# Kernel optimization log

Measured on AMD Instinct MI355X. Metric: run time of the kernel, lower is better.

Reference implementation:

```python
import jax, jax.numpy as jnp
import numpy as np

N, E, H, PIN, PEIN, POUT, L = 50000, 800000, 128, 16, 8, 8, 4
EPS = 1e-7


def setup_inputs() -> dict:
    key = jax.random.key(0)
    ks = jax.random.split(key, 24)
    f = jax.random.normal
    inp = {
        'x': f(ks[0], (N, PIN), jnp.float32),
        'edge_attr': f(ks[1], (E, PEIN), jnp.float32),
        'edge_index': jax.random.randint(ks[2], (2, E), 0, N, jnp.int32),
        # encoders
        'node_W': f(ks[3], (PIN, H)) * (1.0 / np.sqrt(PIN)),
        'node_b': jnp.zeros((H,)),
        'edge_W': f(ks[4], (PEIN, H)) * (1.0 / np.sqrt(PEIN)),
        'edge_b': jnp.zeros((H,)),
        # GENConv params per layer (stacked over L): MLP Linear(H,2H)->LN->ReLU->Linear(2H,H), temp t
        'W1': f(ks[5], (L, H, 2 * H)) * (1.0 / np.sqrt(H)),
        'b1': jnp.zeros((L, 2 * H)),
        'g1': jnp.ones((L, 2 * H)),
        'be1': jnp.zeros((L, 2 * H)),
        'W2': f(ks[6], (L, 2 * H, H)) * (1.0 / np.sqrt(2 * H)),
        'b2': jnp.zeros((L, H)),
        't': jnp.ones((L,)),
        # DeepGCNLayer LayerNorms
        'ng': jnp.ones((L, H)),
        'nb': jnp.zeros((L, H)),
        # output head
        'out_W': f(ks[7], (H, POUT)) * (1.0 / np.sqrt(H)),
        'out_b': jnp.zeros((POUT,)),
    }
    return inp


def _layernorm(x, g, b):
    mu = jnp.mean(x, -1, keepdims=True)
    v = jnp.mean(jnp.square(x - mu), -1, keepdims=True)
    return (x - mu) * jax.lax.rsqrt(v + 1e-5) * g + b


def reference(x, edge_attr, edge_index, node_W, node_b, edge_W, edge_b,
              W1, b1, g1, be1, W2, b2, t, ng, nb, out_W, out_b):
    src, dst = edge_index[0], edge_index[1]

    def genconv(h, e, i):
        # message: relu(x_j + edge_attr) + eps   [E, H]
        msg = jax.nn.relu(h[src] + e) + EPS
        # softmax aggregation over edges per destination node, temperature t[i]
        s = msg * t[i]
        m = jax.ops.segment_max(s, dst, num_segments=N)  # [N, H]
        w = jnp.exp(s - m[dst])
        denom = jax.ops.segment_sum(w, dst, num_segments=N)
        agg = jax.ops.segment_sum(msg * w, dst, num_segments=N)
        agg = jnp.where(denom > 0, agg / jnp.maximum(denom, EPS), 0.0)
        # root add, then 2-layer MLP (Linear -> LN -> ReLU -> Linear)
        z = agg + h
        z = jax.nn.relu(_layernorm(z @ W1[i] + b1[i], g1[i], be1[i]))
        return z @ W2[i] + b2[i]

    h = x @ node_W + node_b                      # node encoder
    e = jax.nn.sigmoid(edge_attr @ edge_W + edge_b)  # edge encoder
    h = genconv(h, e, 0)                         # layers[0].conv only
    for i in range(1, L):                        # res+ blocks
        z = jax.nn.relu(_layernorm(h, ng[i], nb[i]))
        h = h + genconv(z, e, i)
    h = jax.nn.relu(_layernorm(h, ng[0], nb[0]))  # layers[0] norm+act; dropout=eval identity
    return h @ out_W + out_b
```

## Files before the change

kernel.cpp:

```cpp
#include <hip/hip_runtime.h>
#include <hip/hip_bf16.h>

#define NN 50000
#define NE 800000
#define HH 128
#define PIN_ 16
#define PEIN_ 8
#define POUT_ 8
#define LAYERS_ 4
#define EPSM 1e-7f

typedef __bf16 bf16x8 __attribute__((ext_vector_type(8)));
typedef float f32x4 __attribute__((ext_vector_type(4)));

__device__ inline unsigned short f2bf(float f) {
  unsigned int u = __float_as_uint(f);
  u += 0x7FFFu + ((u >> 16) & 1u);
  return (unsigned short)(u >> 16);
}
__device__ inline unsigned int packbf(float lo, float hi) {
  return (unsigned int)f2bf(lo) | ((unsigned int)f2bf(hi) << 16);
}
__device__ inline float bflo(unsigned int p) { return __uint_as_float(p << 16); }
__device__ inline float bfhi(unsigned int p) { return __uint_as_float(p & 0xFFFF0000u); }


__global__ void count_deg_kernel(const int* __restrict__ dst, int* __restrict__ deg) {
  int i = blockIdx.x * blockDim.x + threadIdx.x;
  if (i < NE) atomicAdd(&deg[dst[i]], 1);
}

__global__ __launch_bounds__(1024) void scan_kernel(const int* __restrict__ deg,
                                                    int* __restrict__ row_ptr,
                                                    int* __restrict__ cursor, int n) {
  __shared__ int wsum[16];
  __shared__ int carry_s;
  int t = threadIdx.x;
  int lane = t & 63, wv = t >> 6;
  if (t == 0) carry_s = 0;
  __syncthreads();
  for (int base = 0; base < n; base += 1024) {
    int i = base + t;
    int v = (i < n) ? deg[i] : 0;
    int x = v;
#pragma unroll
    for (int off = 1; off < 64; off <<= 1) {
      int y = __shfl_up(x, off, 64);
      if (lane >= off) x += y;
    }
    if (lane == 63) wsum[wv] = x;
    __syncthreads();
    if (wv == 0 && lane < 16) {
      int s = wsum[lane];
#pragma unroll
      for (int off = 1; off < 16; off <<= 1) {
        int y = __shfl_up(s, off, 16);
        if (lane >= off) s += y;
      }
      wsum[lane] = s;
    }
    __syncthreads();
    int waveExcl = (wv > 0) ? wsum[wv - 1] : 0;
    int carry = carry_s;
    int excl = carry + waveExcl + x - v;
    if (i < n) { row_ptr[i] = excl; cursor[i] = excl; }
    __syncthreads();
    if (t == 1023) carry_s = carry + wsum[15];
    __syncthreads();
  }
  if (t == 0) row_ptr[n] = carry_s;
}

__global__ void scatter_kernel(const int* __restrict__ src, const int* __restrict__ dst,
                               int* __restrict__ cursor, int2* __restrict__ csr) {
  int i = blockIdx.x * blockDim.x + threadIdx.x;
  if (i < NE) {
    int d = dst[i];
    int pos = atomicAdd(&cursor[d], 1);
    csr[pos] = make_int2(src[i], i);
  }
}


__global__ __launch_bounds__(256) void prep_weights_kernel(
    const float* __restrict__ W1, const float* __restrict__ W2,
    unsigned short* __restrict__ W1Tp, unsigned short* __restrict__ W2T) {
  int idx = blockIdx.x * 256 + threadIdx.x;
  if (idx >= LAYERS_ * 256 * 128) return;
  int l = idx >> 15, r = idx & 32767;
  int n = r >> 7, p = r & 127;
  int k = (p >> 1) + ((p & 1) << 6);
  W1Tp[idx] = f2bf(W1[(l << 15) + k * 256 + n]);
  int c = r >> 8, kk = r & 255;
  W2T[idx] = f2bf(W2[(l << 15) + kk * 128 + c]);
}


__global__ __launch_bounds__(64) void node_enc_kernel(const float* __restrict__ x,
                                                      const float* __restrict__ W,
                                                      const float* __restrict__ b,
                                                      float* __restrict__ h,
                                                      unsigned int* __restrict__ hbp) {
  __shared__ float xs[8 * PIN_];
  int f = threadIdx.x;
  float w0[PIN_], w1[PIN_];
#pragma unroll
  for (int k = 0; k < PIN_; ++k) {
    w0[k] = W[k * HH + f];
    w1[k] = W[k * HH + f + 64];
  }
  float b0 = b[f], b1c = b[f + 64];
  int base = blockIdx.x * 8;
  xs[f] = x[(size_t)base * PIN_ + f];
  xs[f + 64] = x[(size_t)base * PIN_ + f + 64];
  __syncthreads();
#pragma unroll
  for (int r = 0; r < 8; ++r) {
    float a0 = b0, a1 = b1c;
#pragma unroll
    for (int k = 0; k < PIN_; ++k) {
      a0 = fmaf(xs[r * PIN_ + k], w0[k], a0);
      a1 = fmaf(xs[r * PIN_ + k], w1[k], a1);
    }
    h[(size_t)(base + r) * HH + f] = a0;
    h[(size_t)(base + r) * HH + f + 64] = a1;
    hbp[(size_t)(base + r) * 64 + f] = packbf(a0, a1);
  }
}


struct AggState { float d0, d1, a0, a1; };

__device__ __forceinline__ void edge_step(float4 A, float4 B, unsigned int zp,
                                          const float* ew0, const float* ew1,
                                          float eb0, float eb1, float t,
                                          AggState& st) {
  float acc0 = eb0, acc1 = eb1;
  acc0 = fmaf(A.x, ew0[0], acc0); acc0 = fmaf(A.y, ew0[1], acc0);
  acc0 = fmaf(A.z, ew0[2], acc0); acc0 = fmaf(A.w, ew0[3], acc0);
  acc0 = fmaf(B.x, ew0[4], acc0); acc0 = fmaf(B.y, ew0[5], acc0);
  acc0 = fmaf(B.z, ew0[6], acc0); acc0 = fmaf(B.w, ew0[7], acc0);
  acc1 = fmaf(A.x, ew1[0], acc1); acc1 = fmaf(A.y, ew1[1], acc1);
  acc1 = fmaf(A.z, ew1[2], acc1); acc1 = fmaf(A.w, ew1[3], acc1);
  acc1 = fmaf(B.x, ew1[4], acc1); acc1 = fmaf(B.y, ew1[5], acc1);
  acc1 = fmaf(B.z, ew1[6], acc1); acc1 = fmaf(B.w, ew1[7], acc1);
  float e0 = __builtin_amdgcn_rcpf(1.f + __expf(-acc0));
  float e1 = __builtin_amdgcn_rcpf(1.f + __expf(-acc1));
  float msg0 = fmaxf(bflo(zp) + e0, 0.f) + EPSM;
  float msg1 = fmaxf(bfhi(zp) + e1, 0.f) + EPSM;
  float w0 = __expf(msg0 * t), w1 = __expf(msg1 * t);
  st.d0 += w0; st.d1 += w1;
  st.a0 = fmaf(msg0, w0, st.a0);
  st.a1 = fmaf(msg1, w1, st.a1);
}

__global__ __launch_bounds__(256) void aggregate_kernel(
    const int* __restrict__ row_ptr, const int2* __restrict__ csr,
    const float* __restrict__ edge_attr, const float* __restrict__ edge_W,
    const float* __restrict__ edge_b, const unsigned int* __restrict__ zpk,
    const float* __restrict__ t_all, int layer, unsigned int* __restrict__ upk) {
  int wv = threadIdx.x >> 6, lane = threadIdx.x & 63;
  int n = blockIdx.x * 4 + wv;
  if (n >= NN) return;
  float ew0[PEIN_], ew1[PEIN_];
#pragma unroll
  for (int k = 0; k < PEIN_; ++k) {
    ew0[k] = edge_W[k * HH + lane];
    ew1[k] = edge_W[k * HH + lane + 64];
  }
  float eb0 = edge_b[lane], eb1 = edge_b[lane + 64];
  float t = t_all[layer];
  int beg = row_ptr[n], end = row_ptr[n + 1];
  unsigned int zs = zpk[(size_t)n * 64 + lane];
  AggState st = {0.f, 0.f, 0.f, 0.f};

  int p = beg;
  for (; p + 4 <= end; p += 4) {
    int2 se0 = csr[p + 0];
    int2 se1 = csr[p + 1];
    int2 se2 = csr[p + 2];
    int2 se3 = csr[p + 3];
    const float4* e0p = (const float4*)(edge_attr + (size_t)se0.y * PEIN_);
    const float4* e1p = (const float4*)(edge_attr + (size_t)se1.y * PEIN_);
    const float4* e2p = (const float4*)(edge_attr + (size_t)se2.y * PEIN_);
    const float4* e3p = (const float4*)(edge_attr + (size_t)se3.y * PEIN_);
    float4 A0 = e0p[0], B0 = e0p[1];
    float4 A1 = e1p[0], B1 = e1p[1];
    float4 A2 = e2p[0], B2 = e2p[1];
    float4 A3 = e3p[0], B3 = e3p[1];
    unsigned int z0 = zpk[(size_t)se0.x * 64 + lane];
    unsigned int z1 = zpk[(size_t)se1.x * 64 + lane];
    unsigned int z2 = zpk[(size_t)se2.x * 64 + lane];
    unsigned int z3 = zpk[(size_t)se3.x * 64 + lane];
    edge_step(A0, B0, z0, ew0, ew1, eb0, eb1, t, st);
    edge_step(A1, B1, z1, ew0, ew1, eb0, eb1, t, st);
    edge_step(A2, B2, z2, ew0, ew1, eb0, eb1, t, st);
    edge_step(A3, B3, z3, ew0, ew1, eb0, eb1, t, st);
  }
  for (; p < end; ++p) {
    int2 se = csr[p];
    const float4* ep = (const float4*)(edge_attr + (size_t)se.y * PEIN_);
    float4 A = ep[0], B = ep[1];
    unsigned int zp = zpk[(size_t)se.x * 64 + lane];
    edge_step(A, B, zp, ew0, ew1, eb0, eb1, t, st);
  }

  float agg0 = (st.d0 > 0.f) ? st.a0 / fmaxf(st.d0, EPSM) : 0.f;
  float agg1 = (st.d1 > 0.f) ? st.a1 / fmaxf(st.d1, EPSM) : 0.f;
  float u0 = agg0 + bflo(zs);
  float u1 = agg1 + bfhi(zs);
  upk[(size_t)n * 64 + lane] = packbf(u0, u1);
}


__global__ __launch_bounds__(256) void mlp_fused_kernel(
    const unsigned int* __restrict__ upk,
    const unsigned short* __restrict__ W1Tp,
    const float* __restrict__ b1v, const float* __restrict__ g1v,
    const float* __restrict__ be1v,
    const unsigned short* __restrict__ W2T,
    const float* __restrict__ b2v,
    const float* __restrict__ res,
    const float* __restrict__ ngv, const float* __restrict__ nbv,
    float* __restrict__ hout, float* __restrict__ zoutf,
    unsigned int* __restrict__ zbp) {
  __shared__ __align__(16) unsigned short Tlds[4 * 4096];
  int wv = threadIdx.x >> 6, lane = threadIdx.x & 63;
  int gw = blockIdx.x * 4 + wv;
  if (gw >= NN / 16) return;
  int row0 = gw * 16;
  int l15 = lane & 15, qg = lane >> 4;
  int co = 4 * qg;
  int sx = (l15 & 7) << 3;
  unsigned short* tl = Tlds + wv * 4096;

  const unsigned short* ub =
      (const unsigned short*)upk + (size_t)(row0 + l15) * HH + qg * 8;
  bf16x8 ufr[4];
#pragma unroll
  for (int kb = 0; kb < 4; ++kb) ufr[kb] = *(const bf16x8*)(ub + kb * 32);
  f32x4 acc1[16];
#pragma unroll
  for (int nb = 0; nb < 16; ++nb) acc1[nb] = (f32x4){0.f, 0.f, 0.f, 0.f};
#pragma unroll
  for (int nb = 0; nb < 16; ++nb) {
#pragma unroll
    for (int kb = 0; kb < 4; ++kb) {
      bf16x8 wf = *(const bf16x8*)(W1Tp + (size_t)(nb * 16 + l15) * HH + kb * 32 + qg * 8);
      acc1[nb] = __builtin_amdgcn_mfma_f32_16x16x32_bf16(wf, ufr[kb], acc1[nb], 0, 0, 0);
    }
  }

  float sum1 = 0.f;
#pragma unroll
  for (int nb = 0; nb < 16; ++nb) {
    float4 bq = *(const float4*)(b1v + nb * 16 + co);
    acc1[nb][0] += bq.x; acc1[nb][1] += bq.y;
    acc1[nb][2] += bq.z; acc1[nb][3] += bq.w;
    sum1 += acc1[nb][0] + acc1[nb][1] + acc1[nb][2] + acc1[nb][3];
  }
  sum1 += __shfl_xor(sum1, 16, 64);
  sum1 += __shfl_xor(sum1, 32, 64);
  float mu1 = sum1 * (1.f / 256.f);
  float sq1 = 0.f;
#pragma unroll
  for (int nb = 0; nb < 16; ++nb)
#pragma unroll
    for (int i = 0; i < 4; ++i) {
      float d = acc1[nb][i] - mu1;
      sq1 = fmaf(d, d, sq1);
    }
  sq1 += __shfl_xor(sq1, 16, 64);
  sq1 += __shfl_xor(sq1, 32, 64);
  float rstd1 = rsqrtf(sq1 * (1.f / 256.f) + 1e-5f);
#pragma unroll
  for (int nb = 0; nb < 16; ++nb) {
    float4 gq = *(const float4*)(g1v + nb * 16 + co);
    float4 eq = *(const float4*)(be1v + nb * 16 + co);
    float t0 = fmaxf(fmaf((acc1[nb][0] - mu1) * rstd1, gq.x, eq.x), 0.f);
    float t1 = fmaxf(fmaf((acc1[nb][1] - mu1) * rstd1, gq.y, eq.y), 0.f);
    float t2 = fmaxf(fmaf((acc1[nb][2] - mu1) * rstd1, gq.z, eq.z), 0.f);
    float t3 = fmaxf(fmaf((acc1[nb][3] - mu1) * rstd1, gq.w, eq.w), 0.f);
    int ad = l15 * 256 + ((nb * 16 + co) ^ sx);
    *(uint2*)(tl + ad) = make_uint2(packbf(t0, t1), packbf(t2, t3));
  }

  f32x4 acc2[8];
#pragma unroll
  for (int nc = 0; nc < 8; ++nc) acc2[nc] = (f32x4){0.f, 0.f, 0.f, 0.f};
#pragma unroll
  for (int kb = 0; kb < 8; ++kb) {
    bf16x8 tf = *(const bf16x8*)(tl + l15 * 256 + ((kb * 32 + qg * 8) ^ sx));
#pragma unroll
    for (int nc = 0; nc < 8; ++nc) {
      bf16x8 wf = *(const bf16x8*)(W2T + (size_t)(nc * 16 + l15) * 256 + kb * 32 + qg * 8);
      acc2[nc] = __builtin_amdgcn_mfma_f32_16x16x32_bf16(wf, tf, acc2[nc], 0, 0, 0);
    }
  }

  size_t rb = (size_t)(row0 + l15) * HH;
  float sum2 = 0.f;
#pragma unroll
  for (int nc = 0; nc < 8; ++nc) {
    float4 bq = *(const float4*)(b2v + nc * 16 + co);
    acc2[nc][0] += bq.x; acc2[nc][1] += bq.y;
    acc2[nc][2] += bq.z; acc2[nc][3] += bq.w;
    if (res) {
      float4 rq = *(const float4*)(res + rb + nc * 16 + co);
      acc2[nc][0] += rq.x; acc2[nc][1] += rq.y;
      acc2[nc][2] += rq.z; acc2[nc][3] += rq.w;
    }
    *(float4*)(hout + rb + nc * 16 + co) =
        make_float4(acc2[nc][0], acc2[nc][1], acc2[nc][2], acc2[nc][3]);
    sum2 += acc2[nc][0] + acc2[nc][1] + acc2[nc][2] + acc2[nc][3];
  }
  sum2 += __shfl_xor(sum2, 16, 64);
  sum2 += __shfl_xor(sum2, 32, 64);
  float mu2 = sum2 * (1.f / 128.f);
  float sq2 = 0.f;
#pragma unroll
  for (int nc = 0; nc < 8; ++nc)
#pragma unroll
    for (int i = 0; i < 4; ++i) {
      float d = acc2[nc][i] - mu2;
      sq2 = fmaf(d, d, sq2);
    }
  sq2 += __shfl_xor(sq2, 16, 64);
  sq2 += __shfl_xor(sq2, 32, 64);
  float rstd2 = rsqrtf(sq2 * (1.f / 128.f) + 1e-5f);
#pragma unroll
  for (int nc = 0; nc < 8; ++nc) {
    float4 gq = *(const float4*)(ngv + nc * 16 + co);
    float4 eq = *(const float4*)(nbv + nc * 16 + co);
    acc2[nc][0] = fmaxf(fmaf((acc2[nc][0] - mu2) * rstd2, gq.x, eq.x), 0.f);
    acc2[nc][1] = fmaxf(fmaf((acc2[nc][1] - mu2) * rstd2, gq.y, eq.y), 0.f);
    acc2[nc][2] = fmaxf(fmaf((acc2[nc][2] - mu2) * rstd2, gq.z, eq.z), 0.f);
    acc2[nc][3] = fmaxf(fmaf((acc2[nc][3] - mu2) * rstd2, gq.w, eq.w), 0.f);
  }
  if (zoutf) {
#pragma unroll
    for (int nc = 0; nc < 8; ++nc)
      *(float4*)(zoutf + rb + nc * 16 + co) =
          make_float4(acc2[nc][0], acc2[nc][1], acc2[nc][2], acc2[nc][3]);
  }
#pragma unroll
  for (int nc = 0; nc < 4; ++nc) {
    *(uint4*)(zbp + (size_t)(row0 + l15) * 64 + nc * 16 + co) =
        make_uint4(packbf(acc2[nc][0], acc2[nc + 4][0]),
                   packbf(acc2[nc][1], acc2[nc + 4][1]),
                   packbf(acc2[nc][2], acc2[nc + 4][2]),
                   packbf(acc2[nc][3], acc2[nc + 4][3]));
  }
}


__global__ __launch_bounds__(256) void out_head_kernel(const float* __restrict__ zf,
                                                       const float* __restrict__ W,
                                                       const float* __restrict__ b,
                                                       float* __restrict__ out) {
  __shared__ float Wl[HH * POUT_];
  int t = threadIdx.x;
  for (int i = t; i < HH * POUT_; i += 256) Wl[i] = W[i];
  __syncthreads();
  int n = blockIdx.x * 32 + (t >> 3);
  int p = t & 7;
  if (n >= NN) return;
  float acc = b[p];
  const float* zr = zf + (size_t)n * HH;
#pragma unroll 8
  for (int k = 0; k < HH; ++k) acc = fmaf(zr[k], Wl[k * POUT_ + p], acc);
  out[(size_t)n * POUT_ + p] = acc;
}


extern "C" void kernel_launch(void* const* d_in, const int* in_sizes, int n_in,
                              void* d_out, int out_size, void* d_ws, size_t ws_size,
                              hipStream_t stream) {
  const float* x = (const float*)d_in[0];
  const float* edge_attr = (const float*)d_in[1];
  const int* edge_index = (const int*)d_in[2];
  const float* node_W = (const float*)d_in[3];
  const float* node_b = (const float*)d_in[4];
  const float* edge_W = (const float*)d_in[5];
  const float* edge_b = (const float*)d_in[6];
  const float* W1 = (const float*)d_in[7];
  const float* b1 = (const float*)d_in[8];
  const float* g1 = (const float*)d_in[9];
  const float* be1 = (const float*)d_in[10];
  const float* W2 = (const float*)d_in[11];
  const float* b2 = (const float*)d_in[12];
  const float* t_all = (const float*)d_in[13];
  const float* ng = (const float*)d_in[14];
  const float* nb = (const float*)d_in[15];
  const float* out_W = (const float*)d_in[16];
  const float* out_b = (const float*)d_in[17];

  const int* src = edge_index;
  const int* dst = edge_index + NE;

  char* w = (char*)d_ws;
  float* h = (float*)w;
  unsigned int* upk = (unsigned int*)(w + 25600000);
  unsigned int* zbp = (unsigned int*)(w + 38400000);
  unsigned int* hbp = (unsigned int*)(w + 51200000);
  float* zf = (float*)(w + 64000000);
  int* deg = (int*)(w + 89600000);
  int* row_ptr = (int*)(w + 89804800);
  int* cursor = (int*)(w + 90009600);
  int2* csr = (int2*)(w + 90214400);
  unsigned short* W1Tp = (unsigned short*)(w + 96614400);
  unsigned short* W2Tb = (unsigned short*)(w + 96876544);

  hipMemsetAsync(deg, 0, NN * sizeof(int), stream);
  count_deg_kernel<<<(NE + 255) / 256, 256, 0, stream>>>(dst, deg);
  scan_kernel<<<1, 1024, 0, stream>>>(deg, row_ptr, cursor, NN);
  scatter_kernel<<<(NE + 255) / 256, 256, 0, stream>>>(src, dst, cursor, csr);
  prep_weights_kernel<<<512, 256, 0, stream>>>(W1, W2, W1Tp, W2Tb);
  node_enc_kernel<<<NN / 8, 64, 0, stream>>>(x, node_W, node_b, h, hbp);

  const int mlp_blocks = (NN / 16 + 3) / 4;
  for (int i = 0; i < LAYERS_; ++i) {
    const unsigned int* zsrc = (i == 0) ? hbp : zbp;
    aggregate_kernel<<<NN / 4, 256, 0, stream>>>(row_ptr, csr, edge_attr, edge_W, edge_b,
                                                 zsrc, t_all, i, upk);
    int zn = (i + 1) % LAYERS_;
    mlp_fused_kernel<<<mlp_blocks, 256, 0, stream>>>(
        upk, W1Tp + (size_t)i * 32768, b1 + i * 256, g1 + i * 256, be1 + i * 256,
        W2Tb + (size_t)i * 32768, b2 + i * HH,
        (i == 0) ? nullptr : h,
        ng + zn * HH, nb + zn * HH, h,
        (i == LAYERS_ - 1) ? zf : nullptr, zbp);
  }
  out_head_kernel<<<(NN + 31) / 32, 256, 0, stream>>>(zf, out_W, out_b, (float*)d_out);
}
```

Before: 1.000 ms.

## Precompute edge encoder once into CSR-ordered bf16 buffer for all layers

Adds an edge_enc_kernel that computes sigmoid(edge_attr @ edge_W + b) once per edge, in CSR (destination-sorted) order, and stores it as packed bf16. A new aggregate kernel then streams these precomputed embeddings and a compact source-index array with software prefetch of the next indices. This replaces the per-layer recomputation of the edge encoder and the random gathers of edge_attr. In exchange it writes and repeatedly reads a buffer of about 200 MB, so the aggregation may become more memory-bandwidth bound. The new path runs only when the workspace is large enough; otherwise the old kernel is used.

```diff
diff --git a/kernel.cpp b/kernel.cpp
--- a/kernel.cpp
+++ b/kernel.cpp
@@ -72,60 +72,94 @@
 }
 
 __global__ void scatter_kernel(const int* __restrict__ src, const int* __restrict__ dst,
-                               int* __restrict__ cursor, int2* __restrict__ csr) {
+                               int* __restrict__ cursor, int2* __restrict__ csr,
+                               int* __restrict__ srcs) {
   int i = blockIdx.x * blockDim.x + threadIdx.x;
   if (i < NE) {
     int d = dst[i];
     int pos = atomicAdd(&cursor[d], 1);
     csr[pos] = make_int2(src[i], i);
-  }
-}
-
-
-__global__ __launch_bounds__(256) void prep_weights_kernel(
-    const float* __restrict__ W1, const float* __restrict__ W2,
-    unsigned short* __restrict__ W1Tp, unsigned short* __restrict__ W2T) {
-  int idx = blockIdx.x * 256 + threadIdx.x;
-  if (idx >= LAYERS_ * 256 * 128) return;
-  int l = idx >> 15, r = idx & 32767;
-  int n = r >> 7, p = r & 127;
-  int k = (p >> 1) + ((p & 1) << 6);
-  W1Tp[idx] = f2bf(W1[(l << 15) + k * 256 + n]);
-  int c = r >> 8, kk = r & 255;
-  W2T[idx] = f2bf(W2[(l << 15) + kk * 128 + c]);
-}
-
-
-__global__ __launch_bounds__(64) void node_enc_kernel(const float* __restrict__ x,
-                                                      const float* __restrict__ W,
-                                                      const float* __restrict__ b,
-                                                      float* __restrict__ h,
-                                                      unsigned int* __restrict__ hbp) {
-  __shared__ float xs[8 * PIN_];
-  int f = threadIdx.x;
-  float w0[PIN_], w1[PIN_];
-#pragma unroll
-  for (int k = 0; k < PIN_; ++k) {
-    w0[k] = W[k * HH + f];
-    w1[k] = W[k * HH + f + 64];
-  }
-  float b0 = b[f], b1c = b[f + 64];
-  int base = blockIdx.x * 8;
-  xs[f] = x[(size_t)base * PIN_ + f];
-  xs[f + 64] = x[(size_t)base * PIN_ + f + 64];
-  __syncthreads();
-#pragma unroll
-  for (int r = 0; r < 8; ++r) {
-    float a0 = b0, a1 = b1c;
-#pragma unroll
-    for (int k = 0; k < PIN_; ++k) {
-      a0 = fmaf(xs[r * PIN_ + k], w0[k], a0);
-      a1 = fmaf(xs[r * PIN_ + k], w1[k], a1);
-    }
-    h[(size_t)(base + r) * HH + f] = a0;
-    h[(size_t)(base + r) * HH + f + 64] = a1;
-    hbp[(size_t)(base + r) * 64 + f] = packbf(a0, a1);
-  }
+    if (srcs) srcs[pos] = src[i];
+  }
+}
+
+
+__global__ __launch_bounds__(256) void edge_enc_kernel(
+    const int2* __restrict__ csr, const float* __restrict__ edge_attr,
+    const float* __restrict__ edge_W, const float* __restrict__ edge_b,
+    unsigned int* __restrict__ epk) {
+  int wv = threadIdx.x >> 6, lane = threadIdx.x & 63;
+  int p = blockIdx.x * 4 + wv;
+  if (p >= NE) return;
+  int2 se = csr[p];
+  const float4* ea = (const float4*)(edge_attr + (size_t)se.y * PEIN_);
+  float4 A = ea[0], B = ea[1];
+  float acc0 = edge_b[lane], acc1 = edge_b[lane + 64];
+#pragma unroll
+  for (int k = 0; k < PEIN_; ++k) {
+    float av = (k < 4) ? ((k == 0) ? A.x : (k == 1) ? A.y : (k == 2) ? A.z : A.w)
+                       : ((k == 4) ? B.x : (k == 5) ? B.y : (k == 6) ? B.z : B.w);
+    acc0 = fmaf(av, edge_W[k * HH + lane], acc0);
+    acc1 = fmaf(av, edge_W[k * HH + lane + 64], acc1);
+  }
+  float e0 = __builtin_amdgcn_rcpf(1.f + __expf(-acc0));
+  float e1 = __builtin_amdgcn_rcpf(1.f + __expf(-acc1));
+  epk[(size_t)p * 64 + lane] = packbf(e0, e1);
+}
+
+
+__device__ __forceinline__ void estep(unsigned int ep, unsigned int zp, float t,
+                                      float& d0, float& d1, float& a0, float& a1) {
+  float msg0 = fmaxf(bflo(zp) + bflo(ep), 0.f) + EPSM;
+  float msg1 = fmaxf(bfhi(zp) + bfhi(ep), 0.f) + EPSM;
+  float w0 = __expf(msg0 * t), w1 = __expf(msg1 * t);
+  d0 += w0; d1 += w1;
+  a0 = fmaf(msg0, w0, a0);
+  a1 = fmaf(msg1, w1, a1);
+}
+
+__global__ __launch_bounds__(256) void aggregate_pre_kernel(
+    const int* __restrict__ row_ptr, const int* __restrict__ srcs,
+    const unsigned int* __restrict__ epk, const unsigned int* __restrict__ zpk,
+    const float* __restrict__ t_all, int layer, unsigned int* __restrict__ upk) {
+  int wv = threadIdx.x >> 6, lane = threadIdx.x & 63;
+  int n = blockIdx.x * 4 + wv;
+  if (n >= NN) return;
+  float t = t_all[layer];
+  int beg = row_ptr[n], end = row_ptr[n + 1];
+  unsigned int zs = zpk[(size_t)n * 64 + lane];
+  float d0 = 0.f, d1 = 0.f, a0 = 0.f, a1 = 0.f;
+
+  int p = beg;
+  if (p + 4 <= end) {
+    int s0 = srcs[p], s1 = srcs[p + 1], s2 = srcs[p + 2], s3 = srcs[p + 3];
+    for (; p + 4 <= end; p += 4) {
+      int n0 = srcs[p + 4], n1 = srcs[p + 5], n2 = srcs[p + 6], n3 = srcs[p + 7];
+      unsigned int z0 = zpk[(size_t)s0 * 64 + lane];
+      unsigned int z1 = zpk[(size_t)s1 * 64 + lane];
+      unsigned int z2 = zpk[(size_t)s2 * 64 + lane];
+      unsigned int z3 = zpk[(size_t)s3 * 64 + lane];
+      unsigned int e0 = epk[(size_t)(p + 0) * 64 + lane];
+      unsigned int e1 = epk[(size_t)(p + 1) * 64 + lane];
+      unsigned int e2 = epk[(size_t)(p + 2) * 64 + lane];
+      unsigned int e3 = epk[(size_t)(p + 3) * 64 + lane];
+      estep(e0, z0, t, d0, d1, a0, a1);
+      estep(e1, z1, t, d0, d1, a0, a1);
+      estep(e2, z2, t, d0, d1, a0, a1);
+      estep(e3, z3, t, d0, d1, a0, a1);
+      s0 = n0; s1 = n1; s2 = n2; s3 = n3;
+    }
+  }
+  for (; p < end; ++p) {
+    int s = srcs[p];
+    unsigned int e = epk[(size_t)p * 64 + lane];
+    unsigned int z = zpk[(size_t)s * 64 + lane];
+    estep(e, z, t, d0, d1, a0, a1);
+  }
+
+  float agg0 = (d0 > 0.f) ? a0 / fmaxf(d0, EPSM) : 0.f;
+  float agg1 = (d1 > 0.f) ? a1 / fmaxf(d1, EPSM) : 0.f;
+  upk[(size_t)n * 64 + lane] = packbf(agg0 + bflo(zs), agg1 + bfhi(zs));
 }
 
 
@@ -173,7 +207,6 @@
   int beg = row_ptr[n], end = row_ptr[n + 1];
   unsigned int zs = zpk[(size_t)n * 64 + lane];
   AggState st = {0.f, 0.f, 0.f, 0.f};
-
   int p = beg;
   for (; p + 4 <= end; p += 4) {
     int2 se0 = csr[p + 0];
@@ -204,12 +237,56 @@
     unsigned int zp = zpk[(size_t)se.x * 64 + lane];
     edge_step(A, B, zp, ew0, ew1, eb0, eb1, t, st);
   }
-
   float agg0 = (st.d0 > 0.f) ? st.a0 / fmaxf(st.d0, EPSM) : 0.f;
   float agg1 = (st.d1 > 0.f) ? st.a1 / fmaxf(st.d1, EPSM) : 0.f;
-  float u0 = agg0 + bflo(zs);
-  float u1 = agg1 + bfhi(zs);
-  upk[(size_t)n * 64 + lane] = packbf(u0, u1);
+  upk[(size_t)n * 64 + lane] = packbf(agg0 + bflo(zs), agg1 + bfhi(zs));
+}
+
+
+__global__ __launch_bounds__(256) void prep_weights_kernel(
+    const float* __restrict__ W1, const float* __restrict__ W2,
+    unsigned short* __restrict__ W1Tp, unsigned short* __restrict__ W2T) {
+  int idx = blockIdx.x * 256 + threadIdx.x;
+  if (idx >= LAYERS_ * 256 * 128) return;
+  int l = idx >> 15, r = idx & 32767;
+  int n = r >> 7, p = r & 127;
+  int k = (p >> 1) + ((p & 1) << 6);
+  W1Tp[idx] = f2bf(W1[(l << 15) + k * 256 + n]);
+  int c = r >> 8, kk = r & 255;
+  W2T[idx] = f2bf(W2[(l << 15) + kk * 128 + c]);
+}
+
+
+__global__ __launch_bounds__(64) void node_enc_kernel(const float* __restrict__ x,
+                                                      const float* __restrict__ W,
+                                                      const float* __restrict__ b,
+                                                      float* __restrict__ h,
+                                                      unsigned int* __restrict__ hbp) {
+  __shared__ float xs[8 * PIN_];
+  int f = threadIdx.x;
+  float w0[PIN_], w1[PIN_];
+#pragma unroll
+  for (int k = 0; k < PIN_; ++k) {
+    w0[k] = W[k * HH + f];
+    w1[k] = W[k * HH + f + 64];
+  }
+  float b0 = b[f], b1c = b[f + 64];
+  int base = blockIdx.x * 8;
+  xs[f] = x[(size_t)base * PIN_ + f];
+  xs[f + 64] = x[(size_t)base * PIN_ + f + 64];
+  __syncthreads();
+#pragma unroll
+  for (int r = 0; r < 8; ++r) {
+    float a0 = b0, a1 = b1c;
+#pragma unroll
+    for (int k = 0; k < PIN_; ++k) {
+      a0 = fmaf(xs[r * PIN_ + k], w0[k], a0);
+      a1 = fmaf(xs[r * PIN_ + k], w1[k], a1);
+    }
+    h[(size_t)(base + r) * HH + f] = a0;
+    h[(size_t)(base + r) * HH + f + 64] = a1;
+    hbp[(size_t)(base + r) * 64 + f] = packbf(a0, a1);
+  }
 }
 
 
@@ -410,19 +487,33 @@
   int2* csr = (int2*)(w + 90214400);
   unsigned short* W1Tp = (unsigned short*)(w + 96614400);
   unsigned short* W2Tb = (unsigned short*)(w + 96876544);
+  int* srcs = (int*)(w + 97200000);
+  unsigned int* epk = (unsigned int*)(w + 100500000);
+  const size_t ws_needed = 100500000ull + (size_t)NE * 256ull;
+  const bool use_epk = ws_size >= ws_needed;
 
   hipMemsetAsync(deg, 0, NN * sizeof(int), stream);
   count_deg_kernel<<<(NE + 255) / 256, 256, 0, stream>>>(dst, deg);
   scan_kernel<<<1, 1024, 0, stream>>>(deg, row_ptr, cursor, NN);
-  scatter_kernel<<<(NE + 255) / 256, 256, 0, stream>>>(src, dst, cursor, csr);
+  scatter_kernel<<<(NE + 255) / 256, 256, 0, stream>>>(src, dst, cursor, csr,
+                                                       use_epk ? srcs : nullptr);
+  if (use_epk) {
+    hipMemsetAsync(srcs + NE, 0, 16 * sizeof(int), stream);
+    edge_enc_kernel<<<NE / 4, 256, 0, stream>>>(csr, edge_attr, edge_W, edge_b, epk);
+  }
   prep_weights_kernel<<<512, 256, 0, stream>>>(W1, W2, W1Tp, W2Tb);
   node_enc_kernel<<<NN / 8, 64, 0, stream>>>(x, node_W, node_b, h, hbp);
 
   const int mlp_blocks = (NN / 16 + 3) / 4;
   for (int i = 0; i < LAYERS_; ++i) {
     const unsigned int* zsrc = (i == 0) ? hbp : zbp;
-    aggregate_kernel<<<NN / 4, 256, 0, stream>>>(row_ptr, csr, edge_attr, edge_W, edge_b,
-                                                 zsrc, t_all, i, upk);
+    if (use_epk) {
+      aggregate_pre_kernel<<<NN / 4, 256, 0, stream>>>(row_ptr, srcs, epk, zsrc,
+                                                       t_all, i, upk);
+    } else {
+      aggregate_kernel<<<NN / 4, 256, 0, stream>>>(row_ptr, csr, edge_attr, edge_W,
+                                                   edge_b, zsrc, t_all, i, upk);
+    }
     int zn = (i + 1) % LAYERS_;
     mlp_fused_kernel<<<mlp_blocks, 256, 0, stream>>>(
         upk, W1Tp + (size_t)i * 32768, b1 + i * 256, g1 + i * 256, be1 + i * 256,
```

Result: no change. 994.7 us (-0.5%).

## Precompute edge encoder once in CSR order and reuse across layers

Applied to the files above, without the earlier changes.

Adds an edge-encoding kernel that computes the sigmoid edge embedding once per edge, in CSR order, and stores it packed as bf16. The per-layer aggregation then streams it instead of recomputing the linear layer and sigmoid each layer. A separate CSR-ordered source-index array is added, and there is a fallback path for edges beyond the available workspace. The fp32 final-activation buffer is also removed so the output head reads bf16 activations. This trades transcendental and FMA work for a large extra memory stream, and lowers the precision of the edge embedding and the head input.

```diff
diff --git a/kernel.cpp b/kernel.cpp
--- a/kernel.cpp
+++ b/kernel.cpp
@@ -12,6 +12,7 @@
 
 typedef __bf16 bf16x8 __attribute__((ext_vector_type(8)));
 typedef float f32x4 __attribute__((ext_vector_type(4)));
+typedef float f32x2 __attribute__((ext_vector_type(2)));
 
 __device__ inline unsigned short f2bf(float f) {
   unsigned int u = __float_as_uint(f);
@@ -23,6 +24,9 @@
 }
 __device__ inline float bflo(unsigned int p) { return __uint_as_float(p << 16); }
 __device__ inline float bfhi(unsigned int p) { return __uint_as_float(p & 0xFFFF0000u); }
+__device__ inline f32x2 unpk(unsigned int p) {
+  return (f32x2){__uint_as_float(p << 16), __uint_as_float(p & 0xFFFF0000u)};
+}
 
 
 __global__ void count_deg_kernel(const int* __restrict__ dst, int* __restrict__ deg) {
@@ -72,13 +76,158 @@
 }
 
 __global__ void scatter_kernel(const int* __restrict__ src, const int* __restrict__ dst,
-                               int* __restrict__ cursor, int2* __restrict__ csr) {
+                               int* __restrict__ cursor, int2* __restrict__ csr,
+                               int* __restrict__ srcs) {
   int i = blockIdx.x * blockDim.x + threadIdx.x;
   if (i < NE) {
     int d = dst[i];
     int pos = atomicAdd(&cursor[d], 1);
     csr[pos] = make_int2(src[i], i);
-  }
+    srcs[pos] = src[i];
+  }
+}
+
+
+__global__ __launch_bounds__(256) void edge_enc_kernel(
+    const int2* __restrict__ csr, const float* __restrict__ edge_attr,
+    const float* __restrict__ edge_W, const float* __restrict__ edge_b,
+    int cap, unsigned int* __restrict__ epk) {
+  int wv = threadIdx.x >> 6, lane = threadIdx.x & 63;
+  int p = blockIdx.x * 4 + wv;
+  if (p >= cap) return;
+  int2 se = csr[p];
+  const float4* ea = (const float4*)(edge_attr + (size_t)se.y * PEIN_);
+  float4 A = ea[0], B = ea[1];
+  float acc0 = edge_b[lane], acc1 = edge_b[lane + 64];
+#pragma unroll
+  for (int k = 0; k < PEIN_; ++k) {
+    float av = (k < 4) ? ((k == 0) ? A.x : (k == 1) ? A.y : (k == 2) ? A.z : A.w)
+                       : ((k == 4) ? B.x : (k == 5) ? B.y : (k == 6) ? B.z : B.w);
+    acc0 = fmaf(av, edge_W[k * HH + lane], acc0);
+    acc1 = fmaf(av, edge_W[k * HH + lane + 64], acc1);
+  }
+  float e0 = __builtin_amdgcn_rcpf(1.f + __expf(-acc0));
+  float e1 = __builtin_amdgcn_rcpf(1.f + __expf(-acc1));
+  epk[(size_t)p * 64 + lane] = packbf(e0, e1);
+}
+
+
+__device__ __forceinline__ void estep(unsigned int ep, unsigned int zp, float t,
+                                      f32x2& d, f32x2& a) {
+  f32x2 msg = unpk(zp) + unpk(ep);
+  msg = __builtin_elementwise_max(msg, (f32x2){0.f, 0.f});
+  msg += (f32x2){EPSM, EPSM};
+  f32x2 s = msg * t;
+  f32x2 w;
+  w.x = __expf(s.x);
+  w.y = __expf(s.y);
+  d += w;
+  a = __builtin_elementwise_fma(msg, w, a);
+}
+
+__device__ __forceinline__ void edge_step(float4 A, float4 B, unsigned int zp,
+                                          const f32x2* ew, f32x2 eb, float t,
+                                          f32x2& d, f32x2& a) {
+  f32x2 acc = eb;
+  acc = __builtin_elementwise_fma((f32x2){A.x, A.x}, ew[0], acc);
+  acc = __builtin_elementwise_fma((f32x2){A.y, A.y}, ew[1], acc);
+  acc = __builtin_elementwise_fma((f32x2){A.z, A.z}, ew[2], acc);
+  acc = __builtin_elementwise_fma((f32x2){A.w, A.w}, ew[3], acc);
+  acc = __builtin_elementwise_fma((f32x2){B.x, B.x}, ew[4], acc);
+  acc = __builtin_elementwise_fma((f32x2){B.y, B.y}, ew[5], acc);
+  acc = __builtin_elementwise_fma((f32x2){B.z, B.z}, ew[6], acc);
+  acc = __builtin_elementwise_fma((f32x2){B.w, B.w}, ew[7], acc);
+  f32x2 e;
+  e.x = __builtin_amdgcn_rcpf(1.f + __expf(-acc.x));
+  e.y = __builtin_amdgcn_rcpf(1.f + __expf(-acc.y));
+  f32x2 msg = unpk(zp) + e;
+  msg = __builtin_elementwise_max(msg, (f32x2){0.f, 0.f});
+  msg += (f32x2){EPSM, EPSM};
+  f32x2 s = msg * t;
+  f32x2 w;
+  w.x = __expf(s.x);
+  w.y = __expf(s.y);
+  d += w;
+  a = __builtin_elementwise_fma(msg, w, a);
+}
+
+__global__ __launch_bounds__(256) void aggregate_hyb_kernel(
+    const int* __restrict__ row_ptr, const int2* __restrict__ csr,
+    const int* __restrict__ srcs, const unsigned int* __restrict__ epk, int cap,
+    const float* __restrict__ edge_attr, const float* __restrict__ edge_W,
+    const float* __restrict__ edge_b, const unsigned int* __restrict__ zpk,
+    const float* __restrict__ t_all, int layer, unsigned int* __restrict__ upk) {
+  int wv = threadIdx.x >> 6, lane = threadIdx.x & 63;
+  int n = blockIdx.x * 4 + wv;
+  if (n >= NN) return;
+  float t = t_all[layer];
+  int beg = row_ptr[n], end = row_ptr[n + 1];
+  unsigned int zs = zpk[(size_t)n * 64 + lane];
+  f32x2 d = {0.f, 0.f}, a = {0.f, 0.f};
+
+  if (end <= cap) {
+    int p = beg;
+    for (; p + 4 <= end; p += 4) {
+      int s0 = srcs[p], s1 = srcs[p + 1], s2 = srcs[p + 2], s3 = srcs[p + 3];
+      unsigned int e0 = epk[(size_t)(p + 0) * 64 + lane];
+      unsigned int e1 = epk[(size_t)(p + 1) * 64 + lane];
+      unsigned int e2 = epk[(size_t)(p + 2) * 64 + lane];
+      unsigned int e3 = epk[(size_t)(p + 3) * 64 + lane];
+      unsigned int z0 = zpk[(size_t)s0 * 64 + lane];
+      unsigned int z1 = zpk[(size_t)s1 * 64 + lane];
+      unsigned int z2 = zpk[(size_t)s2 * 64 + lane];
+      unsigned int z3 = zpk[(size_t)s3 * 64 + lane];
+      estep(e0, z0, t, d, a);
+      estep(e1, z1, t, d, a);
+      estep(e2, z2, t, d, a);
+      estep(e3, z3, t, d, a);
+    }
+    for (; p < end; ++p) {
+      unsigned int e = epk[(size_t)p * 64 + lane];
+      unsigned int z = zpk[(size_t)srcs[p] * 64 + lane];
+      estep(e, z, t, d, a);
+    }
+  } else {
+    f32x2 ew[PEIN_];
+#pragma unroll
+    for (int k = 0; k < PEIN_; ++k)
+      ew[k] = (f32x2){edge_W[k * HH + lane], edge_W[k * HH + lane + 64]};
+    f32x2 eb = (f32x2){edge_b[lane], edge_b[lane + 64]};
+    int p = beg;
+    for (; p + 4 <= end; p += 4) {
+      int2 se0 = csr[p + 0];
+      int2 se1 = csr[p + 1];
+      int2 se2 = csr[p + 2];
+      int2 se3 = csr[p + 3];
+      const float4* e0p = (const float4*)(edge_attr + (size_t)se0.y * PEIN_);
+      const float4* e1p = (const float4*)(edge_attr + (size_t)se1.y * PEIN_);
+      const float4* e2p = (const float4*)(edge_attr + (size_t)se2.y * PEIN_);
+      const float4* e3p = (const float4*)(edge_attr + (size_t)se3.y * PEIN_);
+      float4 A0 = e0p[0], B0 = e0p[1];
+      float4 A1 = e1p[0], B1 = e1p[1];
+      float4 A2 = e2p[0], B2 = e2p[1];
+      float4 A3 = e3p[0], B3 = e3p[1];
+      unsigned int z0 = zpk[(size_t)se0.x * 64 + lane];
+      unsigned int z1 = zpk[(size_t)se1.x * 64 + lane];
+      unsigned int z2 = zpk[(size_t)se2.x * 64 + lane];
+      unsigned int z3 = zpk[(size_t)se3.x * 64 + lane];
+      edge_step(A0, B0, z0, ew, eb, t, d, a);
+      edge_step(A1, B1, z1, ew, eb, t, d, a);
+      edge_step(A2, B2, z2, ew, eb, t, d, a);
+      edge_step(A3, B3, z3, ew, eb, t, d, a);
+    }
+    for (; p < end; ++p) {
+      int2 se = csr[p];
+      const float4* ep = (const float4*)(edge_attr + (size_t)se.y * PEIN_);
+      float4 A = ep[0], B = ep[1];
+      unsigned int zp = zpk[(size_t)se.x * 64 + lane];
+      edge_step(A, B, zp, ew, eb, t, d, a);
+    }
+  }
+
+  float agg0 = (d.x > 0.f) ? a.x / fmaxf(d.x, EPSM) : 0.f;
+  float agg1 = (d.y > 0.f) ? a.y / fmaxf(d.y, EPSM) : 0.f;
+  upk[(size_t)n * 64 + lane] = packbf(agg0 + bflo(zs), agg1 + bfhi(zs));
 }
 
 
@@ -99,7 +248,6 @@
 __global__ __launch_bounds__(64) void node_enc_kernel(const float* __restrict__ x,
                                                       const float* __restrict__ W,
                                                       const float* __restrict__ b,
-                                                      float* __restrict__ h,
                                                       unsigned int* __restrict__ hbp) {
   __shared__ float xs[8 * PIN_];
   int f = threadIdx.x;
@@ -122,94 +270,8 @@
       a0 = fmaf(xs[r * PIN_ + k], w0[k], a0);
       a1 = fmaf(xs[r * PIN_ + k], w1[k], a1);
     }
-    h[(size_t)(base + r) * HH + f] = a0;
-    h[(size_t)(base + r) * HH + f + 64] = a1;
     hbp[(size_t)(base + r) * 64 + f] = packbf(a0, a1);
   }
-}
-
-
-struct AggState { float d0, d1, a0, a1; };
-
-__device__ __forceinline__ void edge_step(float4 A, float4 B, unsigned int zp,
-                                          const float* ew0, const float* ew1,
-                                          float eb0, float eb1, float t,
-                                          AggState& st) {
-  float acc0 = eb0, acc1 = eb1;
-  acc0 = fmaf(A.x, ew0[0], acc0); acc0 = fmaf(A.y, ew0[1], acc0);
-  acc0 = fmaf(A.z, ew0[2], acc0); acc0 = fmaf(A.w, ew0[3], acc0);
-  acc0 = fmaf(B.x, ew0[4], acc0); acc0 = fmaf(B.y, ew0[5], acc0);
-  acc0 = fmaf(B.z, ew0[6], acc0); acc0 = fmaf(B.w, ew0[7], acc0);
-  acc1 = fmaf(A.x, ew1[0], acc1); acc1 = fmaf(A.y, ew1[1], acc1);
-  acc1 = fmaf(A.z, ew1[2], acc1); acc1 = fmaf(A.w, ew1[3], acc1);
-  acc1 = fmaf(B.x, ew1[4], acc1); acc1 = fmaf(B.y, ew1[5], acc1);
-  acc1 = fmaf(B.z, ew1[6], acc1); acc1 = fmaf(B.w, ew1[7], acc1);
-  float e0 = __builtin_amdgcn_rcpf(1.f + __expf(-acc0));
-  float e1 = __builtin_amdgcn_rcpf(1.f + __expf(-acc1));
-  float msg0 = fmaxf(bflo(zp) + e0, 0.f) + EPSM;
-  float msg1 = fmaxf(bfhi(zp) + e1, 0.f) + EPSM;
-  float w0 = __expf(msg0 * t), w1 = __expf(msg1 * t);
-  st.d0 += w0; st.d1 += w1;
-  st.a0 = fmaf(msg0, w0, st.a0);
-  st.a1 = fmaf(msg1, w1, st.a1);
-}
-
-__global__ __launch_bounds__(256) void aggregate_kernel(
-    const int* __restrict__ row_ptr, const int2* __restrict__ csr,
-    const float* __restrict__ edge_attr, const float* __restrict__ edge_W,
-    const float* __restrict__ edge_b, const unsigned int* __restrict__ zpk,
-    const float* __restrict__ t_all, int layer, unsigned int* __restrict__ upk) {
-  int wv = threadIdx.x >> 6, lane = threadIdx.x & 63;
-  int n = blockIdx.x * 4 + wv;
-  if (n >= NN) return;
-  float ew0[PEIN_], ew1[PEIN_];
-#pragma unroll
-  for (int k = 0; k < PEIN_; ++k) {
-    ew0[k] = edge_W[k * HH + lane];
-    ew1[k] = edge_W[k * HH + lane + 64];
-  }
-  float eb0 = edge_b[lane], eb1 = edge_b[lane + 64];
-  float t = t_all[layer];
-  int beg = row_ptr[n], end = row_ptr[n + 1];
-  unsigned int zs = zpk[(size_t)n * 64 + lane];
-  AggState st = {0.f, 0.f, 0.f, 0.f};
-
-  int p = beg;
-  for (; p + 4 <= end; p += 4) {
-    int2 se0 = csr[p + 0];
-    int2 se1 = csr[p + 1];
-    int2 se2 = csr[p + 2];
-    int2 se3 = csr[p + 3];
-    const float4* e0p = (const float4*)(edge_attr + (size_t)se0.y * PEIN_);
-    const float4* e1p = (const float4*)(edge_attr + (size_t)se1.y * PEIN_);
-    const float4* e2p = (const float4*)(edge_attr + (size_t)se2.y * PEIN_);
-    const float4* e3p = (const float4*)(edge_attr + (size_t)se3.y * PEIN_);
-    float4 A0 = e0p[0], B0 = e0p[1];
-    float4 A1 = e1p[0], B1 = e1p[1];
-    float4 A2 = e2p[0], B2 = e2p[1];
-    float4 A3 = e3p[0], B3 = e3p[1];
-    unsigned int z0 = zpk[(size_t)se0.x * 64 + lane];
-    unsigned int z1 = zpk[(size_t)se1.x * 64 + lane];
-    unsigned int z2 = zpk[(size_t)se2.x * 64 + lane];
-    unsigned int z3 = zpk[(size_t)se3.x * 64 + lane];
-    edge_step(A0, B0, z0, ew0, ew1, eb0, eb1, t, st);
-    edge_step(A1, B1, z1, ew0, ew1, eb0, eb1, t, st);
-    edge_step(A2, B2, z2, ew0, ew1, eb0, eb1, t, st);
-    edge_step(A3, B3, z3, ew0, ew1, eb0, eb1, t, st);
-  }
-  for (; p < end; ++p) {
-    int2 se = csr[p];
-    const float4* ep = (const float4*)(edge_attr + (size_t)se.y * PEIN_);
-    float4 A = ep[0], B = ep[1];
-    unsigned int zp = zpk[(size_t)se.x * 64 + lane];
-    edge_step(A, B, zp, ew0, ew1, eb0, eb1, t, st);
-  }
-
-  float agg0 = (st.d0 > 0.f) ? st.a0 / fmaxf(st.d0, EPSM) : 0.f;
-  float agg1 = (st.d1 > 0.f) ? st.a1 / fmaxf(st.d1, EPSM) : 0.f;
-  float u0 = agg0 + bflo(zs);
-  float u1 = agg1 + bfhi(zs);
-  upk[(size_t)n * 64 + lane] = packbf(u0, u1);
 }
 
 
@@ -222,8 +284,7 @@
     const float* __restrict__ b2v,
     const float* __restrict__ res,
     const float* __restrict__ ngv, const float* __restrict__ nbv,
-    float* __restrict__ hout, float* __restrict__ zoutf,
-    unsigned int* __restrict__ zbp) {
+    float* __restrict__ hout, unsigned int* __restrict__ zbp) {
   __shared__ __align__(16) unsigned short Tlds[4 * 4096];
   int wv = threadIdx.x >> 6, lane = threadIdx.x & 63;
   int gw = blockIdx.x * 4 + wv;
@@ -267,8 +328,8 @@
   for (int nb = 0; nb < 16; ++nb)
 #pragma unroll
     for (int i = 0; i < 4; ++i) {
-      float d = acc1[nb][i] - mu1;
-      sq1 = fmaf(d, d, sq1);
+      float dd = acc1[nb][i] - mu1;
+      sq1 = fmaf(dd, dd, sq1);
     }
   sq1 += __shfl_xor(sq1, 16, 64);
   sq1 += __shfl_xor(sq1, 32, 64);
@@ -322,8 +383,8 @@
   for (int nc = 0; nc < 8; ++nc)
 #pragma unroll
     for (int i = 0; i < 4; ++i) {
-      float d = acc2[nc][i] - mu2;
-      sq2 = fmaf(d, d, sq2);
+      float dd = acc2[nc][i] - mu2;
+      sq2 = fmaf(dd, dd, sq2);
     }
   sq2 += __shfl_xor(sq2, 16, 64);
   sq2 += __shfl_xor(sq2, 32, 64);
@@ -337,12 +398,6 @@
     acc2[nc][2] = fmaxf(fmaf((acc2[nc][2] - mu2) * rstd2, gq.z, eq.z), 0.f);
     acc2[nc][3] = fmaxf(fmaf((acc2[nc][3] - mu2) * rstd2, gq.w, eq.w), 0.f);
   }
-  if (zoutf) {
-#pragma unroll
-    for (int nc = 0; nc < 8; ++nc)
-      *(float4*)(zoutf + rb + nc * 16 + co) =
-          make_float4(acc2[nc][0], acc2[nc][1], acc2[nc][2], acc2[nc][3]);
-  }
 #pragma unroll
   for (int nc = 0; nc < 4; ++nc) {
     *(uint4*)(zbp + (size_t)(row0 + l15) * 64 + nc * 16 + co) =
@@ -354,7 +409,7 @@
 }
 
 
-__global__ __launch_bounds__(256) void out_head_kernel(const float* __restrict__ zf,
+__global__ __launch_bounds__(256) void out_head_kernel(const unsigned int* __restrict__ zbp,
                                                        const float* __restrict__ W,
                                                        const float* __restrict__ b,
                                                        float* __restrict__ out) {
@@ -366,9 +421,13 @@
   int p = t & 7;
   if (n >= NN) return;
   float acc = b[p];
-  const float* zr = zf + (size_t)n * HH;
+  const unsigned int* zr = zbp + (size_t)n * 64;
 #pragma unroll 8
-  for (int k = 0; k < HH; ++k) acc = fmaf(zr[k], Wl[k * POUT_ + p], acc);
+  for (int f = 0; f < 64; ++f) {
+    unsigned int zp = zr[f];
+    acc = fmaf(__uint_as_float(zp << 16), Wl[f * POUT_ + p], acc);
+    acc = fmaf(__uint_as_float(zp & 0xFFFF0000u), Wl[(f + 64) * POUT_ + p], acc);
+  }
   out[(size_t)n * POUT_ + p] = acc;
 }
 
@@ -402,34 +461,43 @@
   float* h = (float*)w;
   unsigned int* upk = (unsigned int*)(w + 25600000);
   unsigned int* zbp = (unsigned int*)(w + 38400000);
-  unsigned int* hbp = (unsigned int*)(w + 51200000);
-  float* zf = (float*)(w + 64000000);
-  int* deg = (int*)(w + 89600000);
-  int* row_ptr = (int*)(w + 89804800);
-  int* cursor = (int*)(w + 90009600);
-  int2* csr = (int2*)(w + 90214400);
-  unsigned short* W1Tp = (unsigned short*)(w + 96614400);
-  unsigned short* W2Tb = (unsigned short*)(w + 96876544);
+  int* deg = (int*)(w + 51200000);
+  int* row_ptr = (int*)(w + 51404800);
+  int* cursor = (int*)(w + 51609600);
+  int2* csr = (int2*)(w + 51814400);
+  unsigned short* W1Tp = (unsigned short*)(w + 58214400);
+  unsigned short* W2Tb = (unsigned short*)(w + 58476544);
+  int* srcs = (int*)(w + 58738688);
+  unsigned int* epk = (unsigned int*)(w + 61939200);
+
+  long long avail = (long long)ws_size - 61939200ll;
+  int cap = 0;
+  if (avail > 0) {
+    long long c = avail / 256;
+    cap = (int)(c < (long long)NE ? c : (long long)NE);
+  }
 
   hipMemsetAsync(deg, 0, NN * sizeof(int), stream);
   count_deg_kernel<<<(NE + 255) / 256, 256, 0, stream>>>(dst, deg);
   scan_kernel<<<1, 1024, 0, stream>>>(deg, row_ptr, cursor, NN);
-  scatter_kernel<<<(NE + 255) / 256, 256, 0, stream>>>(src, dst, cursor, csr);
+  scatter_kernel<<<(NE + 255) / 256, 256, 0, stream>>>(src, dst, cursor, csr, srcs);
+  if (cap > 0)
+    edge_enc_kernel<<<(cap + 3) / 4, 256, 0, stream>>>(csr, edge_attr, edge_W, edge_b,
+                                                       cap, epk);
   prep_weights_kernel<<<512, 256, 0, stream>>>(W1, W2, W1Tp, W2Tb);
-  node_enc_kernel<<<NN / 8, 64, 0, stream>>>(x, node_W, node_b, h, hbp);
+  node_enc_kernel<<<NN / 8, 64, 0, stream>>>(x, node_W, node_b, zbp);
 
   const int mlp_blocks = (NN / 16 + 3) / 4;
   for (int i = 0; i < LAYERS_; ++i) {
-    const unsigned int* zsrc = (i == 0) ? hbp : zbp;
-    aggregate_kernel<<<NN / 4, 256, 0, stream>>>(row_ptr, csr, edge_attr, edge_W, edge_b,
-                                                 zsrc, t_all, i, upk);
+    aggregate_hyb_kernel<<<NN / 4, 256, 0, stream>>>(row_ptr, csr, srcs, epk, cap,
+                                                     edge_attr, edge_W, edge_b,
+                                                     zbp, t_all, i, upk);
     int zn = (i + 1) % LAYERS_;
     mlp_fused_kernel<<<mlp_blocks, 256, 0, stream>>>(
         upk, W1Tp + (size_t)i * 32768, b1 + i * 256, g1 + i * 256, be1 + i * 256,
         W2Tb + (size_t)i * 32768, b2 + i * HH,
         (i == 0) ? nullptr : h,
-        ng + zn * HH, nb + zn * HH, h,
-        (i == LAYERS_ - 1) ? zf : nullptr, zbp);
-  }
-  out_head_kernel<<<(NN + 31) / 32, 256, 0, stream>>>(zf, out_W, out_b, (float*)d_out);
-}
+        ng + zn * HH, nb + zn * HH, h, zbp);
+  }
+  out_head_kernel<<<(NN + 31) / 32, 256, 0, stream>>>(zbp, out_W, out_b, (float*)d_out);
+}
```

Result: slower. 1.047 ms (+4.7%).
